# Performance work log

Hardware: AMD Instinct MI355X
Metric: run time of the kernel (lower is better)

The kernel has to match this reference:

```python
import jax, jax.numpy as jnp
import numpy as np

# Physics config (DPhysConfig defaults for the tracked robot)
MASS = 40.0        # robot mass [kg]
GRAV = 9.8         # gravity magnitude
STIFF = 1000.0     # terrain stiffness
DAMP = 100.0       # terrain damping
OMEGA_MAX = 2.0    # angular velocity clamp
DT = 0.01          # integration step [s]
LY = 0.6           # robot width (track separation)
RES = 0.1          # grid resolution [m/cell]


def skew(v):
    # v: (..., 3) -> (..., 3, 3)
    z = jnp.zeros_like(v[..., 0])
    return jnp.stack([
        jnp.stack([z, -v[..., 2], v[..., 1]], -1),
        jnp.stack([v[..., 2], z, -v[..., 0]], -1),
        jnp.stack([-v[..., 1], v[..., 0], z], -1)], -2)


def normalized(x, eps=1e-6):
    return x / jnp.clip(jnp.linalg.norm(x, axis=-1, keepdims=True), eps)


def bilinear(grid, xq, yq):
    # grid: (B, H, W) over [-H*RES/2, H*RES/2] x [-W*RES/2, W*RES/2]; xq, yq: (B, N)
    B, H, W = grid.shape
    u = jnp.clip((xq + H * RES / 2) / RES, 0.0, H - 1.001)
    v = jnp.clip((yq + W * RES / 2) / RES, 0.0, W - 1.001)
    u0 = jnp.floor(u).astype(jnp.int32)
    v0 = jnp.floor(v).astype(jnp.int32)
    du, dv = u - u0, v - v0
    b = jnp.arange(B)[:, None]
    g00 = grid[b, u0, v0]
    g10 = grid[b, u0 + 1, v0]
    g01 = grid[b, u0, v0 + 1]
    g11 = grid[b, u0 + 1, v0 + 1]
    return (g00 * (1 - du) * (1 - dv) + g10 * du * (1 - dv)
            + g01 * (1 - du) * dv + g11 * du * dv)


def inertia_inv(points, mass):
    # points: (N, 3) body-frame point masses -> inverse inertia (3, 3)
    mp = mass / points.shape[0]
    x, y, z = points[:, 0], points[:, 1], points[:, 2]
    Ixx = (mp * (y ** 2 + z ** 2)).sum()
    Iyy = (mp * (x ** 2 + z ** 2)).sum()
    Izz = (mp * (x ** 2 + y ** 2)).sum()
    Ixy = -(mp * x * y).sum()
    Ixz = -(mp * x * z).sum()
    Iyz = -(mp * y * z).sum()
    I = jnp.stack([jnp.stack([Ixx, Ixy, Ixz]),
                   jnp.stack([Ixy, Iyy, Iyz]),
                   jnp.stack([Ixz, Iyz, Izz])])
    return jnp.linalg.inv(I)


def _forward(z_grid, friction, controls, robot_points, x0, xd0, R0, omega0):
    dtype = z_grid.dtype
    I_inv = inertia_inv(robot_points, MASS)          # (3,3), joints fixed -> constant
    gx = jnp.gradient(z_grid, axis=1) / RES          # dz/dx on grid
    gy = jnp.gradient(z_grid, axis=2) / RES          # dz/dy on grid
    maskL = (robot_points[:, 1] < 0).astype(dtype)   # (N,) left track points
    maskR = 1.0 - maskL                              # right track points
    F_grav = MASS * GRAV * jnp.array([0.0, 0.0, -1.0], dtype=dtype)
    clamp = MASS * GRAV

    def dynamics(state, ctrl):
        x, xd, R, omega = state
        # world-frame body points: x_points @ R^T + x
        pts = jnp.einsum('nj,bkj->bnk', robot_points, R) + x[:, None]      # (B,N,3)
        xd_pts = xd[:, None] + jnp.cross(omega[:, None, :], pts - x[:, None], axis=-1)
        px, py = pts[..., 0], pts[..., 1]
        z = bilinear(z_grid, px, py)[..., None]                            # (B,N,1)
        nrm = normalized(jnp.stack([-bilinear(gx, px, py),
                                    -bilinear(gy, px, py),
                                    jnp.ones_like(px)], -1))               # (B,N,3)
        fr = bilinear(friction, px, py)[..., None]                         # (B,N,1)
        dh = pts[..., 2:3] - z
        in_c = jax.nn.sigmoid(-10.0 * dh)
        xd_n = jnp.sum(xd_pts * nrm, -1, keepdims=True)
        F_r = -(STIFF * dh + DAMP * xd_n) * nrm
        F_r = jnp.clip(F_r * in_c / jnp.sum(in_c, 1, keepdims=True), -clamp, clamp)
        thrust = normalized(R[..., 0])                                     # (B,3) first column
        Nmag = jnp.linalg.norm(F_r, axis=2)                                # (B,N)
        v, w = ctrl[:, 0], ctrl[:, 1]
        vL = (v - w * LY / 2)[:, None, None]
        vR = (v + w * LY / 2)[:, None, None]
        cmd = (maskL[None, :, None] * vL + maskR[None, :, None] * vR) * thrust[:, None, :]
        slip = fr * (cmd - xd_pts)
        slip_tau = slip - jnp.sum(slip * nrm, -1, keepdims=True) * nrm
        F_f = jnp.clip(Nmag[..., None] * slip_tau, -clamp, clamp)
        torque = jnp.sum(jnp.cross(pts - x[:, None], F_r + F_f, axis=-1), axis=1)
        omega_d = jnp.clip(torque @ I_inv.T, -OMEGA_MAX, OMEGA_MAX)
        xdd = (F_grav[None] + F_r.sum(1) + F_f.sum(1)) / MASS
        return xdd, omega_d

    def rot_step(R, omega, eps=1e-6):
        # Rodrigues' formula
        Ox = skew(omega)
        th = jnp.linalg.norm(omega, axis=-1)[:, None, None]
        Oxn = Ox / jnp.clip(th, eps)
        I3 = jnp.eye(3, dtype=R.dtype)
        return R @ (I3 + Oxn * jnp.sin(th * DT) + (Oxn @ Oxn) * (1 - jnp.cos(th * DT)))

    def step(state, ctrl):
        x, xd, R, omega = state
        xdd, omega_d = dynamics(state, ctrl)
        xd = xd + xdd * DT          # semi-implicit Euler, as in update_state
        x = x + xd * DT
        omega = omega + omega_d * DT
        R = rot_step(R, omega)
        return (x, xd, R, omega), x

    _, Xs = jax.lax.scan(step, (x0, xd0, R0, omega0), jnp.swapaxes(controls, 0, 1))
    return jnp.swapaxes(Xs, 0, 1)   # (B, T, 3) trajectory positions


def setup_inputs() -> dict:
    key = jax.random.key(0)
    ks = jax.random.split(key, 5)
    B, T, N, H, W = 64, 500, 128, 256, 256
    z_grid = jax.random.uniform(ks[0], (B, H, W), dtype=jnp.float32) * 0.2
    friction = jax.random.uniform(ks[1], (B, H, W), dtype=jnp.float32)
    controls = jax.random.normal(ks[2], (B, T, 2), dtype=jnp.float32) * jnp.array([1.0, 0.5], jnp.float32)
    robot_points = (jax.random.uniform(ks[3], (N, 3), dtype=jnp.float32) - 0.5) \
        * jnp.array([1.0, 0.6, 0.2], jnp.float32)
    x0 = jax.random.normal(ks[4], (B, 3), dtype=jnp.float32) * 0.1 + jnp.array([0.0, 0.0, 0.3], jnp.float32)
    xd0 = jnp.zeros((B, 3), jnp.float32)
    R0 = jnp.tile(jnp.eye(3, dtype=jnp.float32), (B, 1, 1))
    omega0 = jnp.zeros((B, 3), jnp.float32)
    return {"z_grid": z_grid, "friction": friction, "controls": controls,
            "robot_points": robot_points, "x0": x0, "xd0": xd0, "R0": R0, "omega0": omega0}


def reference(z_grid, friction, controls, robot_points, x0, xd0, R0, omega0):
    return _forward(z_grid, friction, controls, robot_points, x0, xd0, R0, omega0)
```

## Files before the change

### kernel.cpp

```cpp
#include <hip/hip_runtime.h>
#include <math.h>

#define GH 256
#define GW 256

typedef float f4 __attribute__((ext_vector_type(4), aligned(4)));
typedef float f2 __attribute__((ext_vector_type(2), aligned(4)));
typedef float f4l __attribute__((ext_vector_type(4)));

template<int CTRL, int RMASK>
__device__ __forceinline__ float dpp_add(float v) {
    int r = __builtin_amdgcn_update_dpp(0, __builtin_bit_cast(int, v), CTRL, RMASK, 0xF, true);
    return v + __builtin_bit_cast(float, r);
}
template<int CTRL, int RMASK>
__device__ __forceinline__ float dpp_max(float v) {
    int r = __builtin_amdgcn_update_dpp(0, __builtin_bit_cast(int, v), CTRL, RMASK, 0xF, true);
    return fmaxf(v, __builtin_bit_cast(float, r));
}
__device__ __forceinline__ float wave_sum63(float v) {
    v = dpp_add<0xB1, 0xF>(v);
    v = dpp_add<0x4E, 0xF>(v);
    v = dpp_add<0x141, 0xF>(v);
    v = dpp_add<0x140, 0xF>(v);
    v = dpp_add<0x142, 0xA>(v);
    v = dpp_add<0x143, 0xC>(v);
    return v;
}
__device__ __forceinline__ float wave_max63(float v) {
    v = dpp_max<0xB1, 0xF>(v);
    v = dpp_max<0x4E, 0xF>(v);
    v = dpp_max<0x141, 0xF>(v);
    v = dpp_max<0x140, 0xF>(v);
    v = dpp_max<0x142, 0xA>(v);
    v = dpp_max<0x143, 0xC>(v);
    return v;
}
__device__ __forceinline__ float rl63(float v) {
    return __builtin_bit_cast(float, __builtin_amdgcn_readlane(__builtin_bit_cast(int, v), 63));
}
__device__ __forceinline__ float frcp(float x)  { return __builtin_amdgcn_rcpf(x); }
__device__ __forceinline__ float frsq(float x)  { return __builtin_amdgcn_rsqf(x); }
__device__ __forceinline__ float fexp2(float x) { return __builtin_amdgcn_exp2f(x); }

__global__ __launch_bounds__(256) void prep_kernel(
    const float* __restrict__ z_grid,
    const float* __restrict__ friction,
    f4* __restrict__ tex)
{
    const int j = threadIdx.x;
    const int i = blockIdx.x;
    const int b = blockIdx.y;
    const float* __restrict__ z = z_grid + (size_t)b * (GH * GW);
    int ipu = (i < GH - 1) ? i + 1 : i;
    int imu = (i > 0) ? i - 1 : i;
    int jpv = (j < GW - 1) ? j + 1 : j;
    int jmv = (j > 0) ? j - 1 : j;
    float scu = (ipu - imu == 2) ? 0.5f : 1.0f;
    float scv = (jpv - jmv == 2) ? 0.5f : 1.0f;
    float gx = ((z[ipu * GW + j] - z[imu * GW + j]) * scu) * 10.0f;
    float gy = ((z[i * GW + jpv] - z[i * GW + jmv]) * scv) * 10.0f;
    f4 o;
    o.x = z[i * GW + j];
    o.y = gx;
    o.z = gy;
    o.w = friction[(size_t)b * (GH * GW) + i * GW + j];
    tex[(size_t)b * (GH * GW) + i * GW + j] = o;
}

__global__ __launch_bounds__(128) void dphys_kernel(
    const f4* __restrict__ tex,
    const float* __restrict__ controls,
    const float* __restrict__ robot_points,
    const float* __restrict__ x0,
    const float* __restrict__ xd0,
    const float* __restrict__ R0,
    const float* __restrict__ omega0,
    float* __restrict__ out,
    int T)
{
    const int b = blockIdx.x;
    const int tid = threadIdx.x;
    const int wv = tid >> 6;
    __shared__ f4l ldsX[2][2][2];
    __shared__ f4l ldsY[2][2];

    const f4* __restrict__ tb = tex + (size_t)b * (GH * GW);
    const float* __restrict__ ct = controls + (size_t)b * (T * 2);
    float* __restrict__ ob = out + (size_t)b * (T * 3);

    const float ppx = robot_points[tid * 3 + 0];
    const float ppy = robot_points[tid * 3 + 1];
    const float ppz = robot_points[tid * 3 + 2];
    const bool isL = (ppy < 0.0f);

    float I6[6];
    I6[0] = ppy * ppy + ppz * ppz;
    I6[1] = ppx * ppx + ppz * ppz;
    I6[2] = ppx * ppx + ppy * ppy;
    I6[3] = ppx * ppy;
    I6[4] = ppx * ppz;
    I6[5] = ppy * ppz;
    #pragma unroll
    for (int k = 0; k < 6; ++k) I6[k] = rl63(wave_sum63(I6[k]));
    if ((tid & 63) == 63) {
        f4l t0; t0.x = I6[0]; t0.y = I6[1]; t0.z = I6[2]; t0.w = I6[3];
        f4l t1; t1.x = I6[4]; t1.y = I6[5]; t1.z = 0.f; t1.w = 0.f;
        ldsY[wv][0] = t0; ldsY[wv][1] = t1;
    }
    __syncthreads();
    {
        f4l o0 = ldsY[wv ^ 1][0], o1 = ldsY[wv ^ 1][1];
        I6[0] += o0.x; I6[1] += o0.y; I6[2] += o0.z;
        I6[3] += o0.w; I6[4] += o1.x; I6[5] += o1.y;
    }
    const float mp = 0.3125f;
    {
        double a = mp * I6[0], bb = mp * I6[1], c = mp * I6[2];
        double d = -(mp * I6[3]), e = -(mp * I6[4]), f = -(mp * I6[5]);
        double C00 = bb * c - f * f, C01 = e * f - d * c, C02 = d * f - bb * e;
        double C11 = a * c - e * e, C12 = d * e - a * f, C22 = a * bb - d * d;
        double idet = 1.0 / (a * C00 + d * C01 + e * C02);
        I6[0] = (float)(C00 * idet); I6[1] = (float)(C11 * idet); I6[2] = (float)(C22 * idet);
        I6[3] = (float)(C01 * idet); I6[4] = (float)(C02 * idet); I6[5] = (float)(C12 * idet);
    }
    const float i00 = I6[0], i11 = I6[1], i22 = I6[2];
    const float i01 = I6[3], i02 = I6[4], i12 = I6[5];

    float X0 = x0[b * 3 + 0], X1 = x0[b * 3 + 1], X2 = x0[b * 3 + 2];
    float V0 = xd0[b * 3 + 0], V1 = xd0[b * 3 + 1], V2 = xd0[b * 3 + 2];
    float W0 = omega0[b * 3 + 0], W1 = omega0[b * 3 + 1], W2 = omega0[b * 3 + 2];
    float R00 = R0[b * 9 + 0], R01 = R0[b * 9 + 1], R02 = R0[b * 9 + 2];
    float R10 = R0[b * 9 + 3], R11 = R0[b * 9 + 4], R12 = R0[b * 9 + 5];
    float R20 = R0[b * 9 + 6], R21 = R0[b * 9 + 7], R22 = R0[b * 9 + 8];

    #pragma unroll 2
    for (int t = 0; t < T; ++t) {
        const int par = t & 1;
        f2 cc = *(const f2*)(ct + t * 2);

        float rx = R00 * ppx + R01 * ppy + R02 * ppz;
        float ry = R10 * ppx + R11 * ppy + R12 * ppz;
        float rz = R20 * ppx + R21 * ppy + R22 * ppz;
        float Px = rx + X0, Py = ry + X1, Pz = rz + X2;
        float l0 = Px - X0, l1 = Py - X1, l2 = Pz - X2;
        float u = (Px + 12.8f) * 10.0f;
        u = fminf(fmaxf(u, 0.0f), 254.999f);
        float vvq = (Py + 12.8f) * 10.0f;
        vvq = fminf(fmaxf(vvq, 0.0f), 254.999f);
        int u0 = (int)u, v0 = (int)vvq;
        int idx = (u0 << 8) + v0;
        f4 c00 = tb[idx];
        f4 c01 = tb[idx + 1];
        f4 c10 = tb[idx + GW];
        f4 c11 = tb[idx + GW + 1];

        float du = u - (float)u0, dv = vvq - (float)v0;
        float w00 = (1.0f - du) * (1.0f - dv);
        float w10 = du * (1.0f - dv);
        float w01 = (1.0f - du) * dv;
        float w11 = du * dv;
        float cv = cc.x, cw = cc.y;
        float half = (cw * 0.6f) * 0.5f;
        float vLs = cv - half, vRs = cv + half;
        float rtn = frsq(R00 * R00 + R10 * R10 + R20 * R20);
        float th0 = R00 * rtn, th1 = R10 * rtn, th2 = R20 * rtn;
        float xp0 = V0 + (W1 * l2 - W2 * l1);
        float xp1 = V1 + (W2 * l0 - W0 * l2);
        float xp2 = V2 + (W0 * l1 - W1 * l0);
        float cmd = isL ? vLs : vRs;
        float ct0 = cmd * th0 - xp0;
        float ct1 = cmd * th1 - xp1;
        float ct2 = cmd * th2 - xp2;

        f4 cb = c00 * w00 + c10 * w10 + c01 * w01 + c11 * w11;
        float zz = cb.x, gxs = cb.y, gys = cb.z, fr = cb.w;

        float rn = frsq(gxs * gxs + gys * gys + 1.0f);
        float nx = -gxs * rn, ny = -gys * rn, nzc = rn;
        float dh = Pz - zz;
        float ex = fexp2(dh * 14.426950408889634f);
        float ic = frcp(1.0f + ex);
        float xdn = xp0 * nx + xp1 * ny + xp2 * nzc;

        float mag = -(1000.0f * dh + 100.0f * xdn);
        float mic = mag * ic;
        float m_abs = fabsf(mic);
        float sl0 = fr * ct0, sl1 = fr * ct1, sl2 = fr * ct2;
        float sdn = sl0 * nx + sl1 * ny + sl2 * nzc;
        float st0 = sl0 - sdn * nx;
        float st1 = sl1 - sdn * ny;
        float st2 = sl2 - sdn * nzc;
        float g0 = mic * nx  + m_abs * st0;
        float g1 = mic * ny  + m_abs * st1;
        float g2 = mic * nzc + m_abs * st2;
        float q0 = l1 * g2 - l2 * g1;
        float q1 = l2 * g0 - l0 * g2;
        float q2 = l0 * g1 - l1 * g0;
        float stm = fmaxf(fmaxf(fabsf(st0), fabsf(st1)), fabsf(st2));
        float worst = fmaxf(stm, 1.0f) * m_abs;

        float d_ic = wave_sum63(ic);
        float d_g0 = wave_sum63(g0), d_g1 = wave_sum63(g1), d_g2 = wave_sum63(g2);
        float d_q0 = wave_sum63(q0), d_q1 = wave_sum63(q1), d_q2 = wave_sum63(q2);
        float d_rw = wave_max63(worst);
        if ((tid & 63) == 63) {
            f4l h0; h0.x = d_g0; h0.y = d_g1; h0.z = d_g2; h0.w = d_q0;
            f4l h1; h1.x = d_q1; h1.y = d_q2; h1.z = d_ic; h1.w = d_rw;
            ldsX[par][wv][0] = h0; ldsX[par][wv][1] = h1;
        }
        float o_ic = rl63(d_ic);
        float o_g0 = rl63(d_g0), o_g1 = rl63(d_g1), o_g2 = rl63(d_g2);
        float o_q0 = rl63(d_q0), o_q1 = rl63(d_q1), o_q2 = rl63(d_q2);
        float o_rw = rl63(d_rw);
        __syncthreads();
        f4l e0 = ldsX[par][wv ^ 1][0], e1 = ldsX[par][wv ^ 1][1];
        float sic = o_ic + e1.z;
        float rwm = fmaxf(o_rw, e1.w);
        float rsic = frcp(sic);

        float FT0, FT1, FT2, TQ0, TQ1, TQ2;
        if (rwm <= 391.0f * sic) {
            FT0 = (o_g0 + e0.x) * rsic;
            FT1 = (o_g1 + e0.y) * rsic;
            FT2 = (o_g2 + e0.z) * rsic;
            TQ0 = (o_q0 + e0.w) * rsic;
            TQ1 = (o_q1 + e1.x) * rsic;
            TQ2 = (o_q2 + e1.y) * rsic;
        } else {
            float s = mic * rsic;
            float Fr0 = fminf(fmaxf(s * nx,  -392.0f), 392.0f);
            float Fr1 = fminf(fmaxf(s * ny,  -392.0f), 392.0f);
            float Fr2 = fminf(fmaxf(s * nzc, -392.0f), 392.0f);
            float Nm = __builtin_amdgcn_sqrtf(Fr0 * Fr0 + Fr1 * Fr1 + Fr2 * Fr2);
            float Ff0 = fminf(fmaxf(Nm * st0, -392.0f), 392.0f);
            float Ff1 = fminf(fmaxf(Nm * st1, -392.0f), 392.0f);
            float Ff2 = fminf(fmaxf(Nm * st2, -392.0f), 392.0f);
            float S0 = Fr0 + Ff0, S1 = Fr1 + Ff1, S2 = Fr2 + Ff2;
            float U0 = l1 * S2 - l2 * S1;
            float U1 = l2 * S0 - l0 * S2;
            float U2 = l0 * S1 - l1 * S0;
            float dS0 = wave_sum63(S0), dS1 = wave_sum63(S1), dS2 = wave_sum63(S2);
            float dU0 = wave_sum63(U0), dU1 = wave_sum63(U1), dU2 = wave_sum63(U2);
            if ((tid & 63) == 63) {
                f4l h0; h0.x = dS0; h0.y = dS1; h0.z = dS2; h0.w = dU0;
                f4l h1; h1.x = dU1; h1.y = dU2; h1.z = 0.f; h1.w = 0.f;
                ldsY[wv][0] = h0; ldsY[wv][1] = h1;
            }
            __syncthreads();
            f4l c0 = ldsY[wv ^ 1][0], c1 = ldsY[wv ^ 1][1];
            FT0 = rl63(dS0) + c0.x; FT1 = rl63(dS1) + c0.y; FT2 = rl63(dS2) + c0.z;
            TQ0 = rl63(dU0) + c0.w; TQ1 = rl63(dU1) + c1.x; TQ2 = rl63(dU2) + c1.y;
        }

        float od0 = fminf(fmaxf(TQ0 * i00 + TQ1 * i01 + TQ2 * i02, -2.0f), 2.0f);
        float od1 = fminf(fmaxf(TQ0 * i01 + TQ1 * i11 + TQ2 * i12, -2.0f), 2.0f);
        float od2 = fminf(fmaxf(TQ0 * i02 + TQ1 * i12 + TQ2 * i22, -2.0f), 2.0f);

        V0 += (FT0 * 0.025f) * 0.01f;
        V1 += (FT1 * 0.025f) * 0.01f;
        V2 += ((-392.0f + FT2) * 0.025f) * 0.01f;
        X0 += V0 * 0.01f; X1 += V1 * 0.01f; X2 += V2 * 0.01f;
        W0 += od0 * 0.01f; W1 += od1 * 0.01f; W2 += od2 * 0.01f;

        if (tid == 0) {
            ob[t * 3 + 0] = X0;
            ob[t * 3 + 1] = X1;
            ob[t * 3 + 2] = X2;
        }

        float th2s = W0 * W0 + W1 * W1 + W2 * W2;
        float a2 = th2s * 1e-4f;
        float s1 = 0.01f - a2 * (0.01f / 6.0f);
        float c2 = 5e-5f - a2 * (1e-4f / 24.0f);
        float w01p = W0 * W1, w02p = W0 * W2, w12p = W1 * W2;
        float A00 = 1.0f - c2 * (W1 * W1 + W2 * W2);
        float A11 = 1.0f - c2 * (W0 * W0 + W2 * W2);
        float A22 = 1.0f - c2 * (W0 * W0 + W1 * W1);
        float A01 = c2 * w01p - s1 * W2;
        float A10 = c2 * w01p + s1 * W2;
        float A02 = c2 * w02p + s1 * W1;
        float A20 = c2 * w02p - s1 * W1;
        float A12 = c2 * w12p - s1 * W0;
        float A21 = c2 * w12p + s1 * W0;
        float N00 = R00 * A00 + R01 * A10 + R02 * A20;
        float N01 = R00 * A01 + R01 * A11 + R02 * A21;
        float N02 = R00 * A02 + R01 * A12 + R02 * A22;
        float N10 = R10 * A00 + R11 * A10 + R12 * A20;
        float N11 = R10 * A01 + R11 * A11 + R12 * A21;
        float N12 = R10 * A02 + R11 * A12 + R12 * A22;
        float N20 = R20 * A00 + R21 * A10 + R22 * A20;
        float N21 = R20 * A01 + R21 * A11 + R22 * A21;
        float N22 = R20 * A02 + R21 * A12 + R22 * A22;
        R00 = N00; R01 = N01; R02 = N02;
        R10 = N10; R11 = N11; R12 = N12;
        R20 = N20; R21 = N21; R22 = N22;
    }
}

__global__ __launch_bounds__(128) void dphys_kernel_fb(
    const float* __restrict__ z_grid,
    const float* __restrict__ friction,
    const float* __restrict__ controls,
    const float* __restrict__ robot_points,
    const float* __restrict__ x0,
    const float* __restrict__ xd0,
    const float* __restrict__ R0,
    const float* __restrict__ omega0,
    float* __restrict__ out,
    int T)
{
    const int b = blockIdx.x;
    const int tid = threadIdx.x;
    const int wv = tid >> 6;
    __shared__ f4l ldsX[2][2][2];
    __shared__ f4l ldsY[2][2];

    const float* __restrict__ zg = z_grid + (size_t)b * (GH * GW);
    const float* __restrict__ fg = friction + (size_t)b * (GH * GW);
    const float* __restrict__ ct = controls + (size_t)b * (T * 2);
    float* __restrict__ ob = out + (size_t)b * (T * 3);

    const float ppx = robot_points[tid * 3 + 0];
    const float ppy = robot_points[tid * 3 + 1];
    const float ppz = robot_points[tid * 3 + 2];
    const bool isL = (ppy < 0.0f);

    float I6[6];
    I6[0] = ppy * ppy + ppz * ppz;
    I6[1] = ppx * ppx + ppz * ppz;
    I6[2] = ppx * ppx + ppy * ppy;
    I6[3] = ppx * ppy;
    I6[4] = ppx * ppz;
    I6[5] = ppy * ppz;
    #pragma unroll
    for (int k = 0; k < 6; ++k) I6[k] = rl63(wave_sum63(I6[k]));
    if ((tid & 63) == 63) {
        f4l t0; t0.x = I6[0]; t0.y = I6[1]; t0.z = I6[2]; t0.w = I6[3];
        f4l t1; t1.x = I6[4]; t1.y = I6[5]; t1.z = 0.f; t1.w = 0.f;
        ldsY[wv][0] = t0; ldsY[wv][1] = t1;
    }
    __syncthreads();
    {
        f4l o0 = ldsY[wv ^ 1][0], o1 = ldsY[wv ^ 1][1];
        I6[0] += o0.x; I6[1] += o0.y; I6[2] += o0.z;
        I6[3] += o0.w; I6[4] += o1.x; I6[5] += o1.y;
    }
    const float mp = 0.3125f;
    {
        double a = mp * I6[0], bb = mp * I6[1], c = mp * I6[2];
        double d = -(mp * I6[3]), e = -(mp * I6[4]), f = -(mp * I6[5]);
        double C00 = bb * c - f * f, C01 = e * f - d * c, C02 = d * f - bb * e;
        double C11 = a * c - e * e, C12 = d * e - a * f, C22 = a * bb - d * d;
        double idet = 1.0 / (a * C00 + d * C01 + e * C02);
        I6[0] = (float)(C00 * idet); I6[1] = (float)(C11 * idet); I6[2] = (float)(C22 * idet);
        I6[3] = (float)(C01 * idet); I6[4] = (float)(C02 * idet); I6[5] = (float)(C12 * idet);
    }
    const float i00 = I6[0], i11 = I6[1], i22 = I6[2];
    const float i01 = I6[3], i02 = I6[4], i12 = I6[5];

    float X0 = x0[b * 3 + 0], X1 = x0[b * 3 + 1], X2 = x0[b * 3 + 2];
    float V0 = xd0[b * 3 + 0], V1 = xd0[b * 3 + 1], V2 = xd0[b * 3 + 2];
    float W0 = omega0[b * 3 + 0], W1 = omega0[b * 3 + 1], W2 = omega0[b * 3 + 2];
    float R00 = R0[b * 9 + 0], R01 = R0[b * 9 + 1], R02 = R0[b * 9 + 2];
    float R10 = R0[b * 9 + 3], R11 = R0[b * 9 + 4], R12 = R0[b * 9 + 5];
    float R20 = R0[b * 9 + 6], R21 = R0[b * 9 + 7], R22 = R0[b * 9 + 8];

    for (int t = 0; t < T; ++t) {
        const int par = t & 1;
        f2 cc = *(const f2*)(ct + t * 2);
        float rx = R00 * ppx + R01 * ppy + R02 * ppz;
        float ry = R10 * ppx + R11 * ppy + R12 * ppz;
        float rz = R20 * ppx + R21 * ppy + R22 * ppz;
        float Px = rx + X0, Py = ry + X1, Pz = rz + X2;
        float l0 = Px - X0, l1 = Py - X1, l2 = Pz - X2;
        float u = (Px + 12.8f) * 10.0f;
        u = fminf(fmaxf(u, 0.0f), 254.999f);
        float vvq = (Py + 12.8f) * 10.0f;
        vvq = fminf(fmaxf(vvq, 0.0f), 254.999f);
        int u0 = (int)u, v0 = (int)vvq;
        bool interior = (u0 >= 1) & (u0 <= 253) & (v0 >= 1) & (v0 <= 253);
        bool fastp = __all(interior);

        float zz, fr, gxs, gys;
        float du = u - (float)u0, dv = vvq - (float)v0;
        float w00 = (1.0f - du) * (1.0f - dv);
        float w10 = du * (1.0f - dv);
        float w01 = (1.0f - du) * dv;
        float w11 = du * dv;

        float cv = cc.x, cw = cc.y;
        float half = (cw * 0.6f) * 0.5f;
        float vLs = cv - half, vRs = cv + half;
        float rtn = frsq(R00 * R00 + R10 * R10 + R20 * R20);
        float th0 = R00 * rtn, th1 = R10 * rtn, th2 = R20 * rtn;
        float xp0 = V0 + (W1 * l2 - W2 * l1);
        float xp1 = V1 + (W2 * l0 - W0 * l2);
        float xp2 = V2 + (W0 * l1 - W1 * l0);
        float cmd = isL ? vLs : vRs;
        float ct0 = cmd * th0 - xp0;
        float ct1 = cmd * th1 - xp1;
        float ct2 = cmd * th2 - xp2;

        if (fastp) {
            int base = (u0 - 1) * GW + (v0 - 1);
            f4 P0 = *(const f4*)(zg + base);
            f4 P1 = *(const f4*)(zg + base + GW);
            f4 P2 = *(const f4*)(zg + base + 2 * GW);
            f4 P3 = *(const f4*)(zg + base + 3 * GW);
            int fb = u0 * GW + v0;
            f2 F0 = *(const f2*)(fg + fb);
            f2 F1 = *(const f2*)(fg + fb + GW);
            zz = P1.y * w00 + P2.y * w10 + P1.z * w01 + P2.z * w11;
            fr = F0.x * w00 + F1.x * w10 + F0.y * w01 + F1.y * w11;
            float gx00 = (P2.y - P0.y) * 5.0f;
            float gx10 = (P3.y - P1.y) * 5.0f;
            float gx01 = (P2.z - P0.z) * 5.0f;
            float gx11 = (P3.z - P1.z) * 5.0f;
            float gy00 = (P1.z - P1.x) * 5.0f;
            float gy10 = (P2.z - P2.x) * 5.0f;
            float gy01 = (P1.w - P1.y) * 5.0f;
            float gy11 = (P2.w - P2.y) * 5.0f;
            gxs = gx00 * w00 + gx10 * w10 + gx01 * w01 + gx11 * w11;
            gys = gy00 * w00 + gy10 * w10 + gy01 * w01 + gy11 * w11;
        } else {
            int basei = u0 * GW + v0;
            zz = zg[basei] * w00 + zg[basei + GW] * w10 + zg[basei + 1] * w01 + zg[basei + GW + 1] * w11;
            fr = fg[basei] * w00 + fg[basei + GW] * w10 + fg[basei + 1] * w01 + fg[basei + GW + 1] * w11;
            float gx[2][2], gy[2][2];
            #pragma unroll
            for (int ii = 0; ii < 2; ++ii) {
                int i = u0 + ii;
                int ipu = (i < GH - 1) ? i + 1 : i;
                int imu = (i > 0) ? i - 1 : i;
                float scu = (ipu - imu == 2) ? 0.5f : 1.0f;
                #pragma unroll
                for (int jj = 0; jj < 2; ++jj) {
                    int j = v0 + jj;
                    int jpv = (j < GW - 1) ? j + 1 : j;
                    int jmv = (j > 0) ? j - 1 : j;
                    float scv = (jpv - jmv == 2) ? 0.5f : 1.0f;
                    gx[ii][jj] = ((zg[ipu * GW + j] - zg[imu * GW + j]) * scu) * 10.0f;
                    gy[ii][jj] = ((zg[i * GW + jpv] - zg[i * GW + jmv]) * scv) * 10.0f;
                }
            }
            gxs = gx[0][0] * w00 + gx[1][0] * w10 + gx[0][1] * w01 + gx[1][1] * w11;
            gys = gy[0][0] * w00 + gy[1][0] * w10 + gy[0][1] * w01 + gy[1][1] * w11;
        }

        float rn = frsq(gxs * gxs + gys * gys + 1.0f);
        float nx = -gxs * rn, ny = -gys * rn, nzc = rn;
        float dh = Pz - zz;
        float ex = fexp2(dh * 14.426950408889634f);
        float ic = frcp(1.0f + ex);
        float xdn = xp0 * nx + xp1 * ny + xp2 * nzc;

        float mag = -(1000.0f * dh + 100.0f * xdn);
        float mic = mag * ic;
        float m_abs = fabsf(mic);
        float sl0 = fr * ct0, sl1 = fr * ct1, sl2 = fr * ct2;
        float sdn = sl0 * nx + sl1 * ny + sl2 * nzc;
        float st0 = sl0 - sdn * nx;
        float st1 = sl1 - sdn * ny;
        float st2 = sl2 - sdn * nzc;
        float g0 = mic * nx  + m_abs * st0;
        float g1 = mic * ny  + m_abs * st1;
        float g2 = mic * nzc + m_abs * st2;
        float q0 = l1 * g2 - l2 * g1;
        float q1 = l2 * g0 - l0 * g2;
        float q2 = l0 * g1 - l1 * g0;
        float stm = fmaxf(fmaxf(fabsf(st0), fabsf(st1)), fabsf(st2));
        float worst = fmaxf(stm, 1.0f) * m_abs;

        float d_ic = wave_sum63(ic);
        float d_g0 = wave_sum63(g0), d_g1 = wave_sum63(g1), d_g2 = wave_sum63(g2);
        float d_q0 = wave_sum63(q0), d_q1 = wave_sum63(q1), d_q2 = wave_sum63(q2);
        float d_rw = wave_max63(worst);
        if ((tid & 63) == 63) {
            f4l h0; h0.x = d_g0; h0.y = d_g1; h0.z = d_g2; h0.w = d_q0;
            f4l h1; h1.x = d_q1; h1.y = d_q2; h1.z = d_ic; h1.w = d_rw;
            ldsX[par][wv][0] = h0; ldsX[par][wv][1] = h1;
        }
        float o_ic = rl63(d_ic);
        float o_g0 = rl63(d_g0), o_g1 = rl63(d_g1), o_g2 = rl63(d_g2);
        float o_q0 = rl63(d_q0), o_q1 = rl63(d_q1), o_q2 = rl63(d_q2);
        float o_rw = rl63(d_rw);
        __syncthreads();
        f4l e0 = ldsX[par][wv ^ 1][0], e1 = ldsX[par][wv ^ 1][1];
        float sic = o_ic + e1.z;
        float rwm = fmaxf(o_rw, e1.w);
        float rsic = frcp(sic);

        float FT0, FT1, FT2, TQ0, TQ1, TQ2;
        if (rwm <= 391.0f * sic) {
            FT0 = (o_g0 + e0.x) * rsic;
            FT1 = (o_g1 + e0.y) * rsic;
            FT2 = (o_g2 + e0.z) * rsic;
            TQ0 = (o_q0 + e0.w) * rsic;
            TQ1 = (o_q1 + e1.x) * rsic;
            TQ2 = (o_q2 + e1.y) * rsic;
        } else {
            float s = mic * rsic;
            float Fr0 = fminf(fmaxf(s * nx,  -392.0f), 392.0f);
            float Fr1 = fminf(fmaxf(s * ny,  -392.0f), 392.0f);
            float Fr2 = fminf(fmaxf(s * nzc, -392.0f), 392.0f);
            float Nm = __builtin_amdgcn_sqrtf(Fr0 * Fr0 + Fr1 * Fr1 + Fr2 * Fr2);
            float Ff0 = fminf(fmaxf(Nm * st0, -392.0f), 392.0f);
            float Ff1 = fminf(fmaxf(Nm * st1, -392.0f), 392.0f);
            float Ff2 = fminf(fmaxf(Nm * st2, -392.0f), 392.0f);
            float S0 = Fr0 + Ff0, S1 = Fr1 + Ff1, S2 = Fr2 + Ff2;
            float U0 = l1 * S2 - l2 * S1;
            float U1 = l2 * S0 - l0 * S2;
            float U2 = l0 * S1 - l1 * S0;
            float dS0 = wave_sum63(S0), dS1 = wave_sum63(S1), dS2 = wave_sum63(S2);
            float dU0 = wave_sum63(U0), dU1 = wave_sum63(U1), dU2 = wave_sum63(U2);
            if ((tid & 63) == 63) {
                f4l h0; h0.x = dS0; h0.y = dS1; h0.z = dS2; h0.w = dU0;
                f4l h1; h1.x = dU1; h1.y = dU2; h1.z = 0.f; h1.w = 0.f;
                ldsY[wv][0] = h0; ldsY[wv][1] = h1;
            }
            __syncthreads();
            f4l c0 = ldsY[wv ^ 1][0], c1 = ldsY[wv ^ 1][1];
            FT0 = rl63(dS0) + c0.x; FT1 = rl63(dS1) + c0.y; FT2 = rl63(dS2) + c0.z;
            TQ0 = rl63(dU0) + c0.w; TQ1 = rl63(dU1) + c1.x; TQ2 = rl63(dU2) + c1.y;
        }

        float od0 = fminf(fmaxf(TQ0 * i00 + TQ1 * i01 + TQ2 * i02, -2.0f), 2.0f);
        float od1 = fminf(fmaxf(TQ0 * i01 + TQ1 * i11 + TQ2 * i12, -2.0f), 2.0f);
        float od2 = fminf(fmaxf(TQ0 * i02 + TQ1 * i12 + TQ2 * i22, -2.0f), 2.0f);

        V0 += (FT0 * 0.025f) * 0.01f;
        V1 += (FT1 * 0.025f) * 0.01f;
        V2 += ((-392.0f + FT2) * 0.025f) * 0.01f;
        X0 += V0 * 0.01f; X1 += V1 * 0.01f; X2 += V2 * 0.01f;
        W0 += od0 * 0.01f; W1 += od1 * 0.01f; W2 += od2 * 0.01f;

        if (tid == 0) {
            ob[t * 3 + 0] = X0;
            ob[t * 3 + 1] = X1;
            ob[t * 3 + 2] = X2;
        }

        float th2s = W0 * W0 + W1 * W1 + W2 * W2;
        float a2 = th2s * 1e-4f;
        float s1 = 0.01f - a2 * (0.01f / 6.0f);
        float c2 = 5e-5f - a2 * (1e-4f / 24.0f);
        float w01p = W0 * W1, w02p = W0 * W2, w12p = W1 * W2;
        float A00 = 1.0f - c2 * (W1 * W1 + W2 * W2);
        float A11 = 1.0f - c2 * (W0 * W0 + W2 * W2);
        float A22 = 1.0f - c2 * (W0 * W0 + W1 * W1);
        float A01 = c2 * w01p - s1 * W2;
        float A10 = c2 * w01p + s1 * W2;
        float A02 = c2 * w02p + s1 * W1;
        float A20 = c2 * w02p - s1 * W1;
        float A12 = c2 * w12p - s1 * W0;
        float A21 = c2 * w12p + s1 * W0;
        float N00 = R00 * A00 + R01 * A10 + R02 * A20;
        float N01 = R00 * A01 + R01 * A11 + R02 * A21;
        float N02 = R00 * A02 + R01 * A12 + R02 * A22;
        float N10 = R10 * A00 + R11 * A10 + R12 * A20;
        float N11 = R10 * A01 + R11 * A11 + R12 * A21;
        float N12 = R10 * A02 + R11 * A12 + R12 * A22;
        float N20 = R20 * A00 + R21 * A10 + R22 * A20;
        float N21 = R20 * A01 + R21 * A11 + R22 * A21;
        float N22 = R20 * A02 + R21 * A12 + R22 * A22;
        R00 = N00; R01 = N01; R02 = N02;
        R10 = N10; R11 = N11; R12 = N12;
        R20 = N20; R21 = N21; R22 = N22;
    }
}

extern "C" void kernel_launch(void* const* d_in, const int* in_sizes, int n_in,
                              void* d_out, int out_size, void* d_ws, size_t ws_size,
                              hipStream_t stream) {
    const float* z_grid       = (const float*)d_in[0];
    const float* friction     = (const float*)d_in[1];
    const float* controls     = (const float*)d_in[2];
    const float* robot_points = (const float*)d_in[3];
    const float* x0           = (const float*)d_in[4];
    const float* xd0          = (const float*)d_in[5];
    const float* R0           = (const float*)d_in[6];
    const float* omega0       = (const float*)d_in[7];
    int B = in_sizes[4] / 3;
    int T = in_sizes[2] / (B * 2);
    size_t need = (size_t)B * GH * GW * sizeof(float) * 4;
    if (ws_size >= need) {
        prep_kernel<<<dim3(GH, B), GW, 0, stream>>>(z_grid, friction, (f4*)d_ws);
        dphys_kernel<<<B, 128, 0, stream>>>((const f4*)d_ws, controls, robot_points,
                                            x0, xd0, R0, omega0, (float*)d_out, T);
    } else {
        dphys_kernel_fb<<<B, 128, 0, stream>>>(z_grid, friction, controls, robot_points,
                                               x0, xd0, R0, omega0, (float*)d_out, T);
    }
}
```

Before: 479.9 us.

## Simulate two batch elements per block to interleave independent dependency chains

Each 128-thread block now advances two batch trajectories at once, interleaving their texture gathers, force math, wave reductions and LDS exchanges so one chain's latency hides behind the other's. It halves the grid to 32 blocks and shares the sync barrier per step across both elements. The kernel is latency-bound per step, so this targets instruction-level parallelism. In exchange it uses more registers, runs on fewer CUs, and the divergent fallback path may add extra barriers per element.

```diff
diff --git a/kernel.cpp b/kernel.cpp
--- a/kernel.cpp
+++ b/kernel.cpp
@@ -68,7 +68,7 @@
     tex[(size_t)b * (GH * GW) + i * GW + j] = o;
 }
 
-__global__ __launch_bounds__(128) void dphys_kernel(
+__global__ __launch_bounds__(128) void dphys_kernel2(
     const f4* __restrict__ tex,
     const float* __restrict__ controls,
     const float* __restrict__ robot_points,
@@ -77,17 +77,24 @@
     const float* __restrict__ R0,
     const float* __restrict__ omega0,
     float* __restrict__ out,
-    int T)
+    int T, int B)
 {
-    const int b = blockIdx.x;
     const int tid = threadIdx.x;
     const int wv = tid >> 6;
-    __shared__ f4l ldsX[2][2][2];
-    __shared__ f4l ldsY[2][2];
-
-    const f4* __restrict__ tb = tex + (size_t)b * (GH * GW);
-    const float* __restrict__ ct = controls + (size_t)b * (T * 2);
-    float* __restrict__ ob = out + (size_t)b * (T * 3);
+    __shared__ f4l ldsX[2][2][2][2];
+    __shared__ f4l ldsY[2][2][2];
+
+    int bb0 = blockIdx.x * 2;
+    int bb1 = bb0 + 1; if (bb1 >= B) bb1 = B - 1;
+    const int bj[2] = {bb0, bb1};
+
+    const f4* tb[2]; const float* ctp[2]; float* obp[2];
+    #pragma unroll
+    for (int j = 0; j < 2; ++j) {
+        tb[j]  = tex + (size_t)bj[j] * (GH * GW);
+        ctp[j] = controls + (size_t)bj[j] * (T * 2);
+        obp[j] = out + (size_t)bj[j] * (T * 3);
+    }
 
     const float ppx = robot_points[tid * 3 + 0];
     const float ppy = robot_points[tid * 3 + 1];
@@ -106,11 +113,11 @@
     if ((tid & 63) == 63) {
         f4l t0; t0.x = I6[0]; t0.y = I6[1]; t0.z = I6[2]; t0.w = I6[3];
         f4l t1; t1.x = I6[4]; t1.y = I6[5]; t1.z = 0.f; t1.w = 0.f;
-        ldsY[wv][0] = t0; ldsY[wv][1] = t1;
+        ldsY[0][wv][0] = t0; ldsY[0][wv][1] = t1;
     }
     __syncthreads();
     {
-        f4l o0 = ldsY[wv ^ 1][0], o1 = ldsY[wv ^ 1][1];
+        f4l o0 = ldsY[0][wv ^ 1][0], o1 = ldsY[0][wv ^ 1][1];
         I6[0] += o0.x; I6[1] += o0.y; I6[2] += o0.z;
         I6[3] += o0.w; I6[4] += o1.x; I6[5] += o1.y;
     }
@@ -127,174 +134,216 @@
     const float i00 = I6[0], i11 = I6[1], i22 = I6[2];
     const float i01 = I6[3], i02 = I6[4], i12 = I6[5];
 
-    float X0 = x0[b * 3 + 0], X1 = x0[b * 3 + 1], X2 = x0[b * 3 + 2];
-    float V0 = xd0[b * 3 + 0], V1 = xd0[b * 3 + 1], V2 = xd0[b * 3 + 2];
-    float W0 = omega0[b * 3 + 0], W1 = omega0[b * 3 + 1], W2 = omega0[b * 3 + 2];
-    float R00 = R0[b * 9 + 0], R01 = R0[b * 9 + 1], R02 = R0[b * 9 + 2];
-    float R10 = R0[b * 9 + 3], R11 = R0[b * 9 + 4], R12 = R0[b * 9 + 5];
-    float R20 = R0[b * 9 + 6], R21 = R0[b * 9 + 7], R22 = R0[b * 9 + 8];
-
-    #pragma unroll 2
+    float X0[2], X1[2], X2[2], V0[2], V1[2], V2[2], W0[2], W1[2], W2[2];
+    float R00[2], R01[2], R02[2], R10[2], R11[2], R12[2], R20[2], R21[2], R22[2];
+    #pragma unroll
+    for (int j = 0; j < 2; ++j) {
+        int b = bj[j];
+        X0[j] = x0[b * 3 + 0]; X1[j] = x0[b * 3 + 1]; X2[j] = x0[b * 3 + 2];
+        V0[j] = xd0[b * 3 + 0]; V1[j] = xd0[b * 3 + 1]; V2[j] = xd0[b * 3 + 2];
+        W0[j] = omega0[b * 3 + 0]; W1[j] = omega0[b * 3 + 1]; W2[j] = omega0[b * 3 + 2];
+        R00[j] = R0[b * 9 + 0]; R01[j] = R0[b * 9 + 1]; R02[j] = R0[b * 9 + 2];
+        R10[j] = R0[b * 9 + 3]; R11[j] = R0[b * 9 + 4]; R12[j] = R0[b * 9 + 5];
+        R20[j] = R0[b * 9 + 6]; R21[j] = R0[b * 9 + 7]; R22[j] = R0[b * 9 + 8];
+    }
+
     for (int t = 0; t < T; ++t) {
         const int par = t & 1;
-        f2 cc = *(const f2*)(ct + t * 2);
-
-        float rx = R00 * ppx + R01 * ppy + R02 * ppz;
-        float ry = R10 * ppx + R11 * ppy + R12 * ppz;
-        float rz = R20 * ppx + R21 * ppy + R22 * ppz;
-        float Px = rx + X0, Py = ry + X1, Pz = rz + X2;
-        float l0 = Px - X0, l1 = Py - X1, l2 = Pz - X2;
-        float u = (Px + 12.8f) * 10.0f;
-        u = fminf(fmaxf(u, 0.0f), 254.999f);
-        float vvq = (Py + 12.8f) * 10.0f;
-        vvq = fminf(fmaxf(vvq, 0.0f), 254.999f);
-        int u0 = (int)u, v0 = (int)vvq;
-        int idx = (u0 << 8) + v0;
-        f4 c00 = tb[idx];
-        f4 c01 = tb[idx + 1];
-        f4 c10 = tb[idx + GW];
-        f4 c11 = tb[idx + GW + 1];
-
-        float du = u - (float)u0, dv = vvq - (float)v0;
-        float w00 = (1.0f - du) * (1.0f - dv);
-        float w10 = du * (1.0f - dv);
-        float w01 = (1.0f - du) * dv;
-        float w11 = du * dv;
-        float cv = cc.x, cw = cc.y;
-        float half = (cw * 0.6f) * 0.5f;
-        float vLs = cv - half, vRs = cv + half;
-        float rtn = frsq(R00 * R00 + R10 * R10 + R20 * R20);
-        float th0 = R00 * rtn, th1 = R10 * rtn, th2 = R20 * rtn;
-        float xp0 = V0 + (W1 * l2 - W2 * l1);
-        float xp1 = V1 + (W2 * l0 - W0 * l2);
-        float xp2 = V2 + (W0 * l1 - W1 * l0);
-        float cmd = isL ? vLs : vRs;
-        float ct0 = cmd * th0 - xp0;
-        float ct1 = cmd * th1 - xp1;
-        float ct2 = cmd * th2 - xp2;
-
-        f4 cb = c00 * w00 + c10 * w10 + c01 * w01 + c11 * w11;
-        float zz = cb.x, gxs = cb.y, gys = cb.z, fr = cb.w;
-
-        float rn = frsq(gxs * gxs + gys * gys + 1.0f);
-        float nx = -gxs * rn, ny = -gys * rn, nzc = rn;
-        float dh = Pz - zz;
-        float ex = fexp2(dh * 14.426950408889634f);
-        float ic = frcp(1.0f + ex);
-        float xdn = xp0 * nx + xp1 * ny + xp2 * nzc;
-
-        float mag = -(1000.0f * dh + 100.0f * xdn);
-        float mic = mag * ic;
-        float m_abs = fabsf(mic);
-        float sl0 = fr * ct0, sl1 = fr * ct1, sl2 = fr * ct2;
-        float sdn = sl0 * nx + sl1 * ny + sl2 * nzc;
-        float st0 = sl0 - sdn * nx;
-        float st1 = sl1 - sdn * ny;
-        float st2 = sl2 - sdn * nzc;
-        float g0 = mic * nx  + m_abs * st0;
-        float g1 = mic * ny  + m_abs * st1;
-        float g2 = mic * nzc + m_abs * st2;
-        float q0 = l1 * g2 - l2 * g1;
-        float q1 = l2 * g0 - l0 * g2;
-        float q2 = l0 * g1 - l1 * g0;
-        float stm = fmaxf(fmaxf(fabsf(st0), fabsf(st1)), fabsf(st2));
-        float worst = fmaxf(stm, 1.0f) * m_abs;
-
-        float d_ic = wave_sum63(ic);
-        float d_g0 = wave_sum63(g0), d_g1 = wave_sum63(g1), d_g2 = wave_sum63(g2);
-        float d_q0 = wave_sum63(q0), d_q1 = wave_sum63(q1), d_q2 = wave_sum63(q2);
-        float d_rw = wave_max63(worst);
+
+        float l0[2], l1[2], l2[2], Pz_[2];
+        float du_[2], dv_[2];
+        f4 c00[2], c01[2], c10[2], c11[2];
+        f2 cc[2];
+        #pragma unroll
+        for (int j = 0; j < 2; ++j) {
+            cc[j] = *(const f2*)(ctp[j] + t * 2);
+            float rx = R00[j] * ppx + R01[j] * ppy + R02[j] * ppz;
+            float ry = R10[j] * ppx + R11[j] * ppy + R12[j] * ppz;
+            float rz = R20[j] * ppx + R21[j] * ppy + R22[j] * ppz;
+            float Px = rx + X0[j], Py = ry + X1[j], Pz = rz + X2[j];
+            l0[j] = Px - X0[j]; l1[j] = Py - X1[j]; l2[j] = Pz - X2[j];
+            Pz_[j] = Pz;
+            float u = (Px + 12.8f) * 10.0f;
+            u = fminf(fmaxf(u, 0.0f), 254.999f);
+            float vv = (Py + 12.8f) * 10.0f;
+            vv = fminf(fmaxf(vv, 0.0f), 254.999f);
+            int u0 = (int)u, v0 = (int)vv;
+            du_[j] = u - (float)u0; dv_[j] = vv - (float)v0;
+            int idx = (u0 << 8) + v0;
+            c00[j] = tb[j][idx];
+            c01[j] = tb[j][idx + 1];
+            c10[j] = tb[j][idx + GW];
+            c11[j] = tb[j][idx + GW + 1];
+        }
+
+        float ic[2], g0[2], g1[2], g2[2], q0[2], q1[2], q2[2], worst[2];
+        float mic[2], nxx[2], nyy[2], nzz[2], st0[2], st1[2], st2[2];
+        #pragma unroll
+        for (int j = 0; j < 2; ++j) {
+            float du = du_[j], dv = dv_[j];
+            float w00 = (1.0f - du) * (1.0f - dv);
+            float w10 = du * (1.0f - dv);
+            float w01 = (1.0f - du) * dv;
+            float w11 = du * dv;
+            float cv = cc[j].x, cw = cc[j].y;
+            float half = (cw * 0.6f) * 0.5f;
+            float vLs = cv - half, vRs = cv + half;
+            float rtn = frsq(R00[j] * R00[j] + R10[j] * R10[j] + R20[j] * R20[j]);
+            float th0 = R00[j] * rtn, th1 = R10[j] * rtn, th2 = R20[j] * rtn;
+            float xp0 = V0[j] + (W1[j] * l2[j] - W2[j] * l1[j]);
+            float xp1 = V1[j] + (W2[j] * l0[j] - W0[j] * l2[j]);
+            float xp2 = V2[j] + (W0[j] * l1[j] - W1[j] * l0[j]);
+            float cmd = isL ? vLs : vRs;
+            float ct0 = cmd * th0 - xp0;
+            float ct1 = cmd * th1 - xp1;
+            float ct2 = cmd * th2 - xp2;
+
+            f4 cb = c00[j] * w00 + c10[j] * w10 + c01[j] * w01 + c11[j] * w11;
+            float zz = cb.x, gxs = cb.y, gys = cb.z, fr = cb.w;
+
+            float rn = frsq(gxs * gxs + gys * gys + 1.0f);
+            float nx = -gxs * rn, ny = -gys * rn, nzc = rn;
+            float dh = Pz_[j] - zz;
+            float ex = fexp2(dh * 14.426950408889634f);
+            float icv = frcp(1.0f + ex);
+            float xdn = xp0 * nx + xp1 * ny + xp2 * nzc;
+
+            float mag = -(1000.0f * dh + 100.0f * xdn);
+            float micv = mag * icv;
+            float m_abs = fabsf(micv);
+            float sl0 = fr * ct0, sl1 = fr * ct1, sl2 = fr * ct2;
+            float sdn = sl0 * nx + sl1 * ny + sl2 * nzc;
+            float s0 = sl0 - sdn * nx;
+            float s1 = sl1 - sdn * ny;
+            float s2 = sl2 - sdn * nzc;
+            float gg0 = micv * nx  + m_abs * s0;
+            float gg1 = micv * ny  + m_abs * s1;
+            float gg2 = micv * nzc + m_abs * s2;
+            ic[j] = icv; mic[j] = micv;
+            nxx[j] = nx; nyy[j] = ny; nzz[j] = nzc;
+            st0[j] = s0; st1[j] = s1; st2[j] = s2;
+            g0[j] = gg0; g1[j] = gg1; g2[j] = gg2;
+            q0[j] = l1[j] * gg2 - l2[j] * gg1;
+            q1[j] = l2[j] * gg0 - l0[j] * gg2;
+            q2[j] = l0[j] * gg1 - l1[j] * gg0;
+            float stm = fmaxf(fmaxf(fabsf(s0), fabsf(s1)), fabsf(s2));
+            worst[j] = fmaxf(stm, 1.0f) * m_abs;
+        }
+
+        float d_ic[2], d_g0[2], d_g1[2], d_g2[2], d_q0[2], d_q1[2], d_q2[2], d_rw[2];
+        #pragma unroll
+        for (int j = 0; j < 2; ++j) {
+            d_ic[j] = wave_sum63(ic[j]);
+            d_g0[j] = wave_sum63(g0[j]);
+            d_g1[j] = wave_sum63(g1[j]);
+            d_g2[j] = wave_sum63(g2[j]);
+            d_q0[j] = wave_sum63(q0[j]);
+            d_q1[j] = wave_sum63(q1[j]);
+            d_q2[j] = wave_sum63(q2[j]);
+            d_rw[j] = wave_max63(worst[j]);
+        }
         if ((tid & 63) == 63) {
-            f4l h0; h0.x = d_g0; h0.y = d_g1; h0.z = d_g2; h0.w = d_q0;
-            f4l h1; h1.x = d_q1; h1.y = d_q2; h1.z = d_ic; h1.w = d_rw;
-            ldsX[par][wv][0] = h0; ldsX[par][wv][1] = h1;
-        }
-        float o_ic = rl63(d_ic);
-        float o_g0 = rl63(d_g0), o_g1 = rl63(d_g1), o_g2 = rl63(d_g2);
-        float o_q0 = rl63(d_q0), o_q1 = rl63(d_q1), o_q2 = rl63(d_q2);
-        float o_rw = rl63(d_rw);
+            #pragma unroll
+            for (int j = 0; j < 2; ++j) {
+                f4l h0; h0.x = d_g0[j]; h0.y = d_g1[j]; h0.z = d_g2[j]; h0.w = d_q0[j];
+                f4l h1; h1.x = d_q1[j]; h1.y = d_q2[j]; h1.z = d_ic[j]; h1.w = d_rw[j];
+                ldsX[par][j][wv][0] = h0; ldsX[par][j][wv][1] = h1;
+            }
+        }
+        float o_ic[2], o_g0[2], o_g1[2], o_g2[2], o_q0[2], o_q1[2], o_q2[2], o_rw[2];
+        #pragma unroll
+        for (int j = 0; j < 2; ++j) {
+            o_ic[j] = rl63(d_ic[j]);
+            o_g0[j] = rl63(d_g0[j]); o_g1[j] = rl63(d_g1[j]); o_g2[j] = rl63(d_g2[j]);
+            o_q0[j] = rl63(d_q0[j]); o_q1[j] = rl63(d_q1[j]); o_q2[j] = rl63(d_q2[j]);
+            o_rw[j] = rl63(d_rw[j]);
+        }
         __syncthreads();
-        f4l e0 = ldsX[par][wv ^ 1][0], e1 = ldsX[par][wv ^ 1][1];
-        float sic = o_ic + e1.z;
-        float rwm = fmaxf(o_rw, e1.w);
-        float rsic = frcp(sic);
-
-        float FT0, FT1, FT2, TQ0, TQ1, TQ2;
-        if (rwm <= 391.0f * sic) {
-            FT0 = (o_g0 + e0.x) * rsic;
-            FT1 = (o_g1 + e0.y) * rsic;
-            FT2 = (o_g2 + e0.z) * rsic;
-            TQ0 = (o_q0 + e0.w) * rsic;
-            TQ1 = (o_q1 + e1.x) * rsic;
-            TQ2 = (o_q2 + e1.y) * rsic;
-        } else {
-            float s = mic * rsic;
-            float Fr0 = fminf(fmaxf(s * nx,  -392.0f), 392.0f);
-            float Fr1 = fminf(fmaxf(s * ny,  -392.0f), 392.0f);
-            float Fr2 = fminf(fmaxf(s * nzc, -392.0f), 392.0f);
-            float Nm = __builtin_amdgcn_sqrtf(Fr0 * Fr0 + Fr1 * Fr1 + Fr2 * Fr2);
-            float Ff0 = fminf(fmaxf(Nm * st0, -392.0f), 392.0f);
-            float Ff1 = fminf(fmaxf(Nm * st1, -392.0f), 392.0f);
-            float Ff2 = fminf(fmaxf(Nm * st2, -392.0f), 392.0f);
-            float S0 = Fr0 + Ff0, S1 = Fr1 + Ff1, S2 = Fr2 + Ff2;
-            float U0 = l1 * S2 - l2 * S1;
-            float U1 = l2 * S0 - l0 * S2;
-            float U2 = l0 * S1 - l1 * S0;
-            float dS0 = wave_sum63(S0), dS1 = wave_sum63(S1), dS2 = wave_sum63(S2);
-            float dU0 = wave_sum63(U0), dU1 = wave_sum63(U1), dU2 = wave_sum63(U2);
-            if ((tid & 63) == 63) {
-                f4l h0; h0.x = dS0; h0.y = dS1; h0.z = dS2; h0.w = dU0;
-                f4l h1; h1.x = dU1; h1.y = dU2; h1.z = 0.f; h1.w = 0.f;
-                ldsY[wv][0] = h0; ldsY[wv][1] = h1;
+
+        #pragma unroll
+        for (int j = 0; j < 2; ++j) {
+            f4l e0 = ldsX[par][j][wv ^ 1][0], e1 = ldsX[par][j][wv ^ 1][1];
+            float sic = o_ic[j] + e1.z;
+            float rwm = fmaxf(o_rw[j], e1.w);
+            float rsic = frcp(sic);
+
+            float FT0, FT1, FT2, TQ0, TQ1, TQ2;
+            if (rwm <= 391.0f * sic) {
+                FT0 = (o_g0[j] + e0.x) * rsic;
+                FT1 = (o_g1[j] + e0.y) * rsic;
+                FT2 = (o_g2[j] + e0.z) * rsic;
+                TQ0 = (o_q0[j] + e0.w) * rsic;
+                TQ1 = (o_q1[j] + e1.x) * rsic;
+                TQ2 = (o_q2[j] + e1.y) * rsic;
+            } else {
+                float s = mic[j] * rsic;
+                float Fr0 = fminf(fmaxf(s * nxx[j], -392.0f), 392.0f);
+                float Fr1 = fminf(fmaxf(s * nyy[j], -392.0f), 392.0f);
+                float Fr2 = fminf(fmaxf(s * nzz[j], -392.0f), 392.0f);
+                float Nm = __builtin_amdgcn_sqrtf(Fr0 * Fr0 + Fr1 * Fr1 + Fr2 * Fr2);
+                float Ff0 = fminf(fmaxf(Nm * st0[j], -392.0f), 392.0f);
+                float Ff1 = fminf(fmaxf(Nm * st1[j], -392.0f), 392.0f);
+                float Ff2 = fminf(fmaxf(Nm * st2[j], -392.0f), 392.0f);
+                float S0 = Fr0 + Ff0, S1 = Fr1 + Ff1, S2 = Fr2 + Ff2;
+                float U0 = l1[j] * S2 - l2[j] * S1;
+                float U1 = l2[j] * S0 - l0[j] * S2;
+                float U2 = l0[j] * S1 - l1[j] * S0;
+                float dS0 = wave_sum63(S0), dS1 = wave_sum63(S1), dS2 = wave_sum63(S2);
+                float dU0 = wave_sum63(U0), dU1 = wave_sum63(U1), dU2 = wave_sum63(U2);
+                if ((tid & 63) == 63) {
+                    f4l h0; h0.x = dS0; h0.y = dS1; h0.z = dS2; h0.w = dU0;
+                    f4l h1; h1.x = dU1; h1.y = dU2; h1.z = 0.f; h1.w = 0.f;
+                    ldsY[j][wv][0] = h0; ldsY[j][wv][1] = h1;
+                }
+                __syncthreads();
+                f4l c0 = ldsY[j][wv ^ 1][0], c1 = ldsY[j][wv ^ 1][1];
+                FT0 = rl63(dS0) + c0.x; FT1 = rl63(dS1) + c0.y; FT2 = rl63(dS2) + c0.z;
+                TQ0 = rl63(dU0) + c0.w; TQ1 = rl63(dU1) + c1.x; TQ2 = rl63(dU2) + c1.y;
             }
-            __syncthreads();
-            f4l c0 = ldsY[wv ^ 1][0], c1 = ldsY[wv ^ 1][1];
-            FT0 = rl63(dS0) + c0.x; FT1 = rl63(dS1) + c0.y; FT2 = rl63(dS2) + c0.z;
-            TQ0 = rl63(dU0) + c0.w; TQ1 = rl63(dU1) + c1.x; TQ2 = rl63(dU2) + c1.y;
-        }
-
-        float od0 = fminf(fmaxf(TQ0 * i00 + TQ1 * i01 + TQ2 * i02, -2.0f), 2.0f);
-        float od1 = fminf(fmaxf(TQ0 * i01 + TQ1 * i11 + TQ2 * i12, -2.0f), 2.0f);
-        float od2 = fminf(fmaxf(TQ0 * i02 + TQ1 * i12 + TQ2 * i22, -2.0f), 2.0f);
-
-        V0 += (FT0 * 0.025f) * 0.01f;
-        V1 += (FT1 * 0.025f) * 0.01f;
-        V2 += ((-392.0f + FT2) * 0.025f) * 0.01f;
-        X0 += V0 * 0.01f; X1 += V1 * 0.01f; X2 += V2 * 0.01f;
-        W0 += od0 * 0.01f; W1 += od1 * 0.01f; W2 += od2 * 0.01f;
-
-        if (tid == 0) {
-            ob[t * 3 + 0] = X0;
-            ob[t * 3 + 1] = X1;
-            ob[t * 3 + 2] = X2;
-        }
-
-        float th2s = W0 * W0 + W1 * W1 + W2 * W2;
-        float a2 = th2s * 1e-4f;
-        float s1 = 0.01f - a2 * (0.01f / 6.0f);
-        float c2 = 5e-5f - a2 * (1e-4f / 24.0f);
-        float w01p = W0 * W1, w02p = W0 * W2, w12p = W1 * W2;
-        float A00 = 1.0f - c2 * (W1 * W1 + W2 * W2);
-        float A11 = 1.0f - c2 * (W0 * W0 + W2 * W2);
-        float A22 = 1.0f - c2 * (W0 * W0 + W1 * W1);
-        float A01 = c2 * w01p - s1 * W2;
-        float A10 = c2 * w01p + s1 * W2;
-        float A02 = c2 * w02p + s1 * W1;
-        float A20 = c2 * w02p - s1 * W1;
-        float A12 = c2 * w12p - s1 * W0;
-        float A21 = c2 * w12p + s1 * W0;
-        float N00 = R00 * A00 + R01 * A10 + R02 * A20;
-        float N01 = R00 * A01 + R01 * A11 + R02 * A21;
-        float N02 = R00 * A02 + R01 * A12 + R02 * A22;
-        float N10 = R10 * A00 + R11 * A10 + R12 * A20;
-        float N11 = R10 * A01 + R11 * A11 + R12 * A21;
-        float N12 = R10 * A02 + R11 * A12 + R12 * A22;
-        float N20 = R20 * A00 + R21 * A10 + R22 * A20;
-        float N21 = R20 * A01 + R21 * A11 + R22 * A21;
-        float N22 = R20 * A02 + R21 * A12 + R22 * A22;
-        R00 = N00; R01 = N01; R02 = N02;
-        R10 = N10; R11 = N11; R12 = N12;
-        R20 = N20; R21 = N21; R22 = N22;
+
+            float od0 = fminf(fmaxf(TQ0 * i00 + TQ1 * i01 + TQ2 * i02, -2.0f), 2.0f);
+            float od1 = fminf(fmaxf(TQ0 * i01 + TQ1 * i11 + TQ2 * i12, -2.0f), 2.0f);
+            float od2 = fminf(fmaxf(TQ0 * i02 + TQ1 * i12 + TQ2 * i22, -2.0f), 2.0f);
+
+            V0[j] += (FT0 * 0.025f) * 0.01f;
+            V1[j] += (FT1 * 0.025f) * 0.01f;
+            V2[j] += ((-392.0f + FT2) * 0.025f) * 0.01f;
+            X0[j] += V0[j] * 0.01f; X1[j] += V1[j] * 0.01f; X2[j] += V2[j] * 0.01f;
+            W0[j] += od0 * 0.01f; W1[j] += od1 * 0.01f; W2[j] += od2 * 0.01f;
+
+            if (tid == 0) {
+                obp[j][t * 3 + 0] = X0[j];
+                obp[j][t * 3 + 1] = X1[j];
+                obp[j][t * 3 + 2] = X2[j];
+            }
+
+            float th2s = W0[j] * W0[j] + W1[j] * W1[j] + W2[j] * W2[j];
+            float a2 = th2s * 1e-4f;
+            float s1r = 0.01f - a2 * (0.01f / 6.0f);
+            float c2r = 5e-5f - a2 * (1e-4f / 24.0f);
+            float w01p = W0[j] * W1[j], w02p = W0[j] * W2[j], w12p = W1[j] * W2[j];
+            float A00 = 1.0f - c2r * (W1[j] * W1[j] + W2[j] * W2[j]);
+            float A11 = 1.0f - c2r * (W0[j] * W0[j] + W2[j] * W2[j]);
+            float A22 = 1.0f - c2r * (W0[j] * W0[j] + W1[j] * W1[j]);
+            float A01 = c2r * w01p - s1r * W2[j];
+            float A10 = c2r * w01p + s1r * W2[j];
+            float A02 = c2r * w02p + s1r * W1[j];
+            float A20 = c2r * w02p - s1r * W1[j];
+            float A12 = c2r * w12p - s1r * W0[j];
+            float A21 = c2r * w12p + s1r * W0[j];
+            float N00 = R00[j] * A00 + R01[j] * A10 + R02[j] * A20;
+            float N01 = R00[j] * A01 + R01[j] * A11 + R02[j] * A21;
+            float N02 = R00[j] * A02 + R01[j] * A12 + R02[j] * A22;
+            float N10 = R10[j] * A00 + R11[j] * A10 + R12[j] * A20;
+            float N11 = R10[j] * A01 + R11[j] * A11 + R12[j] * A21;
+            float N12 = R10[j] * A02 + R11[j] * A12 + R12[j] * A22;
+            float N20 = R20[j] * A00 + R21[j] * A10 + R22[j] * A20;
+            float N21 = R20[j] * A01 + R21[j] * A11 + R22[j] * A21;
+            float N22 = R20[j] * A02 + R21[j] * A12 + R22[j] * A22;
+            R00[j] = N00; R01[j] = N01; R02[j] = N02;
+            R10[j] = N10; R11[j] = N11; R12[j] = N12;
+            R20[j] = N20; R21[j] = N21; R22[j] = N22;
+        }
     }
 }
 
@@ -586,8 +635,9 @@
     size_t need = (size_t)B * GH * GW * sizeof(float) * 4;
     if (ws_size >= need) {
         prep_kernel<<<dim3(GH, B), GW, 0, stream>>>(z_grid, friction, (f4*)d_ws);
-        dphys_kernel<<<B, 128, 0, stream>>>((const f4*)d_ws, controls, robot_points,
-                                            x0, xd0, R0, omega0, (float*)d_out, T);
+        int nb = (B + 1) / 2;
+        dphys_kernel2<<<nb, 128, 0, stream>>>((const f4*)d_ws, controls, robot_points,
+                                              x0, xd0, R0, omega0, (float*)d_out, T, B);
     } else {
         dphys_kernel_fb<<<B, 128, 0, stream>>>(z_grid, friction, controls, robot_points,
                                                x0, xd0, R0, omega0, (float*)d_out, T);
```

Result: slower. 915.9 us (+90.9%).
